# Kernel tuning notes

Measured on AMD Instinct MI355X. Metric: run time of the kernel, lower is better.

The kernel has to match this reference:

```python
import jax, jax.numpy as jnp
import numpy as np

B, C, H, W, K = 4, 32, 64, 64, 64
BH, BW = 2, 2  # block_size
RF_THRESH = 0.05  # gaussian support threshold (lattice kernels are ~0 outside RF)


def _gaussian_lattice(key, n_kernels, h, w):
    """Build Gaussian receptive-field kernels like lattice.gaussian_kernel_lattice:
    rfs[k,i,j] = exp(-((i-mu_y)^2 + (j-mu_x)^2) / (2*sigma^2)), thresholded to
    zero outside the RF so each kernel has compact support."""
    k1, k2 = jax.random.split(key)
    mu = jax.random.uniform(k1, (n_kernels, 2), minval=8.0, maxval=h - 8.0)
    sigma = jax.random.uniform(k2, (n_kernels, 1), minval=4.0, maxval=7.0)
    yy = jnp.arange(h, dtype=jnp.float32)[:, None]
    xx = jnp.arange(w, dtype=jnp.float32)[None, :]
    d2 = (yy[None] - mu[:, 0, None, None]) ** 2 + (xx[None] - mu[:, 1, None, None]) ** 2
    g = jnp.exp(-d2 / (2.0 * sigma[:, :, None] ** 2))  # (K, h, w)
    return jnp.where(g > RF_THRESH, g, 0.0).astype(jnp.float32)


def setup_inputs() -> dict:
    key = jax.random.key(0)
    ku, kr = jax.random.split(key)
    u = jax.random.normal(ku, (B, C, H, W), dtype=jnp.float32)
    rfs = _gaussian_lattice(kr, K, H, W)
    return {"u": u, "rfs": rfs}


def reference(u, rfs):
    """RF_Pool.__call__ with pool_type='prob', block_size=(2,2): returns p_mean.

    For each receptive field k, the kernel is elementwise-multiplied with u and
    a probabilistic max-pool (Lee et al.) with an 'off' state is computed over
    the RF support:  h_mean_k = exp(u*rf_k) / (1 + sum_{RF_k} exp(u*rf_k)).
    Detection probabilities are accumulated over RFs, then pooling-unit means
    p_mean are taken as the block-wise max over block_size blocks."""
    dt = u.dtype
    mask = rfs > 0  # (K, H, W) RF supports
    neg = jnp.asarray(-1e30, dt)
    # kernel-weighted pre-activations per RF: (B, C, K, H, W)
    v = u[:, :, None, :, :] * rfs[None, None]
    vm = jnp.where(mask[None, None], v, neg)
    # stable normalization including the off-state exp(0)=1
    m = jnp.maximum(jnp.max(vm, axis=(-2, -1), keepdims=True), 0.0)
    e = jnp.where(mask[None, None], jnp.exp(v - m), 0.0)
    denom = jnp.exp(-m) + jnp.sum(e, axis=(-2, -1), keepdims=True)
    h_mean = jnp.sum(e / denom, axis=2)  # (B, C, H, W) sum over RFs
    # block-wise pooling to p_mean: (B, C, H//BH, W//BW)
    p_mean = h_mean.reshape(B, C, H // BH, BH, W // BW, BW).max(axis=(3, 5))
    return p_mean
```

## Files before the change

kernel.cpp:

```cpp
#include <hip/hip_runtime.h>
#include <hip/hip_bf16.h>

#define BB 4
#define CC 32
#define HH 64
#define WW 64
#define KK 64
#define PIX (HH * WW)
#define NBC (BB * CC)

__global__ __launch_bounds__(256) void rf_phase1(
        const float* __restrict__ u,
        const float* __restrict__ rfs,
        float2* __restrict__ mk) {
    const int bc = blockIdx.x >> 3;
    const int kg = blockIdx.x & 7;
    const int t  = threadIdx.x;
    const int w  = t >> 6;
    const int l  = t & 63;

    __shared__ float su[PIX];
    {
        const float4* u4  = (const float4*)(u + (size_t)bc * PIX);
        float4*       su4 = (float4*)su;
        #pragma unroll
        for (int i = 0; i < 4; ++i) su4[t + 256 * i] = u4[t + 256 * i];
    }
    __syncthreads();

    const float4* su4 = (const float4*)su;

    #pragma unroll
    for (int kk = 0; kk < 2; ++kk) {
        const int k = kg * 8 + kk * 4 + w;
        const float4* r4 = (const float4*)(rfs + (size_t)k * PIX);

        float mloc = 0.f;
        #pragma unroll
        for (int i = 0; i < 16; ++i) {
            const float4 rv = r4[64 * i + l];
            const float4 uv = su4[64 * i + l];
            if (rv.x > 0.f) mloc = fmaxf(mloc, uv.x * rv.x);
            if (rv.y > 0.f) mloc = fmaxf(mloc, uv.y * rv.y);
            if (rv.z > 0.f) mloc = fmaxf(mloc, uv.z * rv.z);
            if (rv.w > 0.f) mloc = fmaxf(mloc, uv.w * rv.w);
        }
        #pragma unroll
        for (int off = 32; off > 0; off >>= 1)
            mloc = fmaxf(mloc, __shfl_xor(mloc, off, 64));
        const float m = mloc;

        float s = 0.f;
        #pragma unroll
        for (int i = 0; i < 16; ++i) {
            const float4 rv = r4[64 * i + l];
            const float4 uv = su4[64 * i + l];
            if (rv.x > 0.f) s += __expf(uv.x * rv.x - m);
            if (rv.y > 0.f) s += __expf(uv.y * rv.y - m);
            if (rv.z > 0.f) s += __expf(uv.z * rv.z - m);
            if (rv.w > 0.f) s += __expf(uv.w * rv.w - m);
        }
        #pragma unroll
        for (int off = 32; off > 0; off >>= 1)
            s += __shfl_xor(s, off, 64);

        if (l == 0)
            mk[bc * KK + k] = make_float2(m, 1.f / (__expf(-m) + s));
    }
}

__global__ __launch_bounds__(256) void rf_phase2(
        const float* __restrict__ u,
        const float* __restrict__ rfs,
        const float2* __restrict__ mk,
        float* __restrict__ out) {
    const int bc    = blockIdx.x >> 2;
    const int chunk = blockIdx.x & 3;
    const int t     = threadIdx.x;
    const int pbase = chunk * 1024;

    __shared__ float2 smk[KK];
    __shared__ float  hm[16 * 33];

    if (t < KK) smk[t] = mk[bc * KK + t];

    const float4 uv = ((const float4*)(u + (size_t)bc * PIX + pbase))[t];
    __syncthreads();

    float4 h = make_float4(0.f, 0.f, 0.f, 0.f);
    for (int k = 0; k < KK; ++k) {
        const float4 rv = ((const float4*)(rfs + (size_t)k * PIX + pbase))[t];
        const float2 MI = smk[k];
        if (rv.x > 0.f) h.x += __expf(uv.x * rv.x - MI.x) * MI.y;
        if (rv.y > 0.f) h.y += __expf(uv.y * rv.y - MI.x) * MI.y;
        if (rv.z > 0.f) h.z += __expf(uv.z * rv.z - MI.x) * MI.y;
        if (rv.w > 0.f) h.w += __expf(uv.w * rv.w - MI.x) * MI.y;
    }

    const int row = t >> 4;
    const int c2  = (t & 15) * 2;
    hm[row * 33 + c2]     = fmaxf(h.x, h.y);
    hm[row * 33 + c2 + 1] = fmaxf(h.z, h.w);
    __syncthreads();

    const int orow = t >> 5;
    const int ocol = t & 31;
    const float r = fmaxf(hm[(2 * orow) * 33 + ocol],
                          hm[(2 * orow + 1) * 33 + ocol]);
    out[(size_t)bc * (HH / 2) * (WW / 2) + (chunk * 8 + orow) * 32 + ocol] = r;
}

extern "C" void kernel_launch(void* const* d_in, const int* in_sizes, int n_in,
                              void* d_out, int out_size, void* d_ws, size_t ws_size,
                              hipStream_t stream) {
    const float* u   = (const float*)d_in[0];
    const float* rfs = (const float*)d_in[1];
    float* out       = (float*)d_out;
    float2* mk       = (float2*)d_ws;

    rf_phase1<<<NBC * 8, 256, 0, stream>>>(u, rfs, mk);
    rf_phase2<<<NBC * 4, 256, 0, stream>>>(u, rfs, mk, out);
}
```

Measured before the change: 89.54 us.

## Drop max-subtraction pass and remap phase2 to per-row scalar threads

Phase 1 drops the max-reduction pass and computes exp(u*rf) directly, normalizing with 1/(1+sum). This is valid because the exponent is bounded for these inputs (rf<=1, u normal), so one pass over rfs and one reduction are removed. Phase 1 now launches one k per wave (twice as many blocks), and phase 2 uses scalar loads of two rows per thread with a shuffle-based 2x2 max instead of shared memory. The change loses overflow safety for large u and issues narrower, less vectorized loads.

```diff
diff --git a/kernel.cpp b/kernel.cpp
--- a/kernel.cpp
+++ b/kernel.cpp
@@ -9,12 +9,13 @@
 #define PIX (HH * WW)
 #define NBC (BB * CC)
 
+
 __global__ __launch_bounds__(256) void rf_phase1(
         const float* __restrict__ u,
         const float* __restrict__ rfs,
-        float2* __restrict__ mk) {
-    const int bc = blockIdx.x >> 3;
-    const int kg = blockIdx.x & 7;
+        float* __restrict__ inv) {
+    const int bc = blockIdx.x >> 4;
+    const int kg = blockIdx.x & 15;
     const int t  = threadIdx.x;
     const int w  = t >> 6;
     const int l  = t & 63;
@@ -28,86 +29,62 @@
     }
     __syncthreads();
 
+    const int k = kg * 4 + w;
+    const float4* r4  = (const float4*)(rfs + (size_t)k * PIX);
     const float4* su4 = (const float4*)su;
 
+    float s = 0.f;
     #pragma unroll
-    for (int kk = 0; kk < 2; ++kk) {
-        const int k = kg * 8 + kk * 4 + w;
-        const float4* r4 = (const float4*)(rfs + (size_t)k * PIX);
+    for (int i = 0; i < 16; ++i) {
+        const float4 rv = r4[64 * i + l];
+        const float4 uv = su4[64 * i + l];
+        const float ex = __expf(uv.x * rv.x);
+        const float ey = __expf(uv.y * rv.y);
+        const float ez = __expf(uv.z * rv.z);
+        const float ew = __expf(uv.w * rv.w);
+        s += (rv.x > 0.f) ? ex : 0.f;
+        s += (rv.y > 0.f) ? ey : 0.f;
+        s += (rv.z > 0.f) ? ez : 0.f;
+        s += (rv.w > 0.f) ? ew : 0.f;
+    }
+    #pragma unroll
+    for (int off = 32; off > 0; off >>= 1)
+        s += __shfl_xor(s, off, 64);
 
-        float mloc = 0.f;
-        #pragma unroll
-        for (int i = 0; i < 16; ++i) {
-            const float4 rv = r4[64 * i + l];
-            const float4 uv = su4[64 * i + l];
-            if (rv.x > 0.f) mloc = fmaxf(mloc, uv.x * rv.x);
-            if (rv.y > 0.f) mloc = fmaxf(mloc, uv.y * rv.y);
-            if (rv.z > 0.f) mloc = fmaxf(mloc, uv.z * rv.z);
-            if (rv.w > 0.f) mloc = fmaxf(mloc, uv.w * rv.w);
-        }
-        #pragma unroll
-        for (int off = 32; off > 0; off >>= 1)
-            mloc = fmaxf(mloc, __shfl_xor(mloc, off, 64));
-        const float m = mloc;
-
-        float s = 0.f;
-        #pragma unroll
-        for (int i = 0; i < 16; ++i) {
-            const float4 rv = r4[64 * i + l];
-            const float4 uv = su4[64 * i + l];
-            if (rv.x > 0.f) s += __expf(uv.x * rv.x - m);
-            if (rv.y > 0.f) s += __expf(uv.y * rv.y - m);
-            if (rv.z > 0.f) s += __expf(uv.z * rv.z - m);
-            if (rv.w > 0.f) s += __expf(uv.w * rv.w - m);
-        }
-        #pragma unroll
-        for (int off = 32; off > 0; off >>= 1)
-            s += __shfl_xor(s, off, 64);
-
-        if (l == 0)
-            mk[bc * KK + k] = make_float2(m, 1.f / (__expf(-m) + s));
-    }
+    if (l == 0) inv[bc * KK + k] = 1.f / (1.f + s);
 }
 
 __global__ __launch_bounds__(256) void rf_phase2(
         const float* __restrict__ u,
         const float* __restrict__ rfs,
-        const float2* __restrict__ mk,
+        const float* __restrict__ inv,
         float* __restrict__ out) {
-    const int bc    = blockIdx.x >> 2;
-    const int chunk = blockIdx.x & 3;
-    const int t     = threadIdx.x;
-    const int pbase = chunk * 1024;
+    const int bc = blockIdx.x >> 3;
+    const int rp = (blockIdx.x & 7) * 4 + (threadIdx.x >> 6);
+    const int l  = threadIdx.x & 63;
 
-    __shared__ float2 smk[KK];
-    __shared__ float  hm[16 * 33];
+    const int pbase = rp * 128 + l;
+    const float u0 = u[(size_t)bc * PIX + pbase];
+    const float u1 = u[(size_t)bc * PIX + pbase + 64];
+    const float* __restrict__ invp = inv + bc * KK;
+    const float* __restrict__ rfp  = rfs + pbase;
 
-    if (t < KK) smk[t] = mk[bc * KK + t];
-
-    const float4 uv = ((const float4*)(u + (size_t)bc * PIX + pbase))[t];
-    __syncthreads();
-
-    float4 h = make_float4(0.f, 0.f, 0.f, 0.f);
+    float h0 = 0.f, h1 = 0.f;
+    #pragma unroll 8
     for (int k = 0; k < KK; ++k) {
-        const float4 rv = ((const float4*)(rfs + (size_t)k * PIX + pbase))[t];
-        const float2 MI = smk[k];
-        if (rv.x > 0.f) h.x += __expf(uv.x * rv.x - MI.x) * MI.y;
-        if (rv.y > 0.f) h.y += __expf(uv.y * rv.y - MI.x) * MI.y;
-        if (rv.z > 0.f) h.z += __expf(uv.z * rv.z - MI.x) * MI.y;
-        if (rv.w > 0.f) h.w += __expf(uv.w * rv.w - MI.x) * MI.y;
+        const float r0 = rfp[(size_t)k * PIX];
+        const float r1 = rfp[(size_t)k * PIX + 64];
+        const float fi = invp[k];
+        const float e0 = __expf(u0 * r0);
+        const float e1 = __expf(u1 * r1);
+        h0 += (r0 > 0.f) ? e0 * fi : 0.f;
+        h1 += (r1 > 0.f) ? e1 * fi : 0.f;
     }
 
-    const int row = t >> 4;
-    const int c2  = (t & 15) * 2;
-    hm[row * 33 + c2]     = fmaxf(h.x, h.y);
-    hm[row * 33 + c2 + 1] = fmaxf(h.z, h.w);
-    __syncthreads();
-
-    const int orow = t >> 5;
-    const int ocol = t & 31;
-    const float r = fmaxf(hm[(2 * orow) * 33 + ocol],
-                          hm[(2 * orow + 1) * 33 + ocol]);
-    out[(size_t)bc * (HH / 2) * (WW / 2) + (chunk * 8 + orow) * 32 + ocol] = r;
+    const float v = fmaxf(h0, h1);
+    const float o = fmaxf(v, __shfl_xor(v, 1, 64));
+    if ((l & 1) == 0)
+        out[(size_t)bc * (HH / 2) * (WW / 2) + rp * 32 + (l >> 1)] = o;
 }
 
 extern "C" void kernel_launch(void* const* d_in, const int* in_sizes, int n_in,
@@ -116,8 +93,8 @@
     const float* u   = (const float*)d_in[0];
     const float* rfs = (const float*)d_in[1];
     float* out       = (float*)d_out;
-    float2* mk       = (float2*)d_ws;
+    float* inv       = (float*)d_ws;
 
-    rf_phase1<<<NBC * 8, 256, 0, stream>>>(u, rfs, mk);
-    rf_phase2<<<NBC * 4, 256, 0, stream>>>(u, rfs, mk, out);
+    rf_phase1<<<NBC * 16, 256, 0, stream>>>(u, rfs, inv);
+    rf_phase2<<<NBC * 8, 256, 0, stream>>>(u, rfs, inv, out);
 }
```

Measured after the change: 73.92 us. 17.4% less time.
